# Optimization experiments

Hardware: AMD Instinct MI355X
Metric: run time of the kernel (lower is better)

## Reference

```python
import jax, jax.numpy as jnp
import numpy as np

N_P = 100000
N_A = 100000
IN = 128
H = 4
D = 32
E = 500000
ALPHA = 0.2


def _leaky(x, a=ALPHA):
    return jnp.where(x > 0, x, a * x)


def _gat_relation(Wh_src_rel, Wh_dst_self, a_src, a_dst, src, dst, n_dst):
    # Wh_src_rel: [Ns,H,D] relation-transformed source feats
    # Wh_dst_self: [Nd,H,D] self-transformed dest feats
    # a_src, a_dst: [H,D] attention vectors; src/dst: [E] edge index
    es = jnp.einsum('nhd,hd->nh', Wh_src_rel, a_src)  # [Ns,H]
    ed = jnp.einsum('nhd,hd->nh', Wh_dst_self, a_dst)  # [Nd,H]
    e = _leaky(es[src] + ed[dst])                      # [E,H]
    m = jax.ops.segment_max(e, dst, num_segments=n_dst)
    m = jnp.where(jnp.isfinite(m), m, 0.0)             # empty segments
    m = jax.lax.stop_gradient(m)
    ee = jnp.exp(e - m[dst])
    s = jax.ops.segment_sum(ee, dst, num_segments=n_dst)
    a = ee / s[dst]                                    # edge_softmax [E,H]
    msg = Wh_src_rel[src] * a[:, :, None]              # [E,H,D]
    return jax.ops.segment_sum(msg, dst, num_segments=n_dst)  # [Nd,H,D]


def setup_inputs() -> dict:
    key = jax.random.key(0)
    ks = jax.random.split(key, 32)
    inp = {
        'feat_P': jax.random.normal(ks[0], (N_P, IN), jnp.float32),
        'feat_A': jax.random.normal(ks[1], (N_A, IN), jnp.float32),
    }
    names = ['p2p', 'p2a', 'a2p', 'a2a']
    nsrc = {'p2p': N_P, 'p2a': N_P, 'a2p': N_A, 'a2a': N_A}
    ndst = {'p2p': N_P, 'p2a': N_A, 'a2p': N_P, 'a2a': N_A}
    for i, r in enumerate(names):
        inp['src_' + r] = jax.random.randint(ks[2 + 2 * i], (E,), 0, nsrc[r], jnp.int32)
        inp['dst_' + r] = jax.random.randint(ks[3 + 2 * i], (E,), 0, ndst[r], jnp.int32)
    # linear weights (torch Linear: y = x @ W.T + b); store as [IN, H*D]
    sc = 1.0 / np.sqrt(IN)
    for i, nm in enumerate(['P', 'A', 'p2p', 'p2a', 'a2p', 'a2a']):
        inp['W_' + nm] = jax.random.uniform(ks[10 + i], (IN, H * D), jnp.float32, -sc, sc)
        inp['b_' + nm] = jax.random.uniform(ks[16 + i], (H * D,), jnp.float32, -sc, sc)
    # attention vectors [H,D]
    for i, nm in enumerate(['p2p_src', 'p2p_dst', 'p2a_src', 'p2a_dst',
                            'a2p_src', 'a2p_dst', 'a2a_src', 'a2a_dst']):
        inp['att_' + nm] = jax.random.normal(ks[22 + i], (H, D), jnp.float32) * 0.1
    return inp


def reference(feat_P, feat_A,
              src_p2p, dst_p2p, src_p2a, dst_p2a,
              src_a2p, dst_a2p, src_a2a, dst_a2a,
              W_P, b_P, W_A, b_A, W_p2p, b_p2p, W_p2a, b_p2a,
              W_a2p, b_a2p, W_a2a, b_a2a,
              att_p2p_src, att_p2p_dst, att_p2a_src, att_p2a_dst,
              att_a2p_src, att_a2p_dst, att_a2a_src, att_a2a_dst):
    lin = lambda x, W, b: (x @ W + b).reshape(-1, H, D)
    Whp = lin(feat_P, W_P, b_P)      # [N_P,H,D]
    Wha = lin(feat_A, W_A, b_A)      # [N_A,H,D]
    Whp2p = lin(feat_P, W_p2p, b_p2p)
    Whp2a = lin(feat_P, W_p2a, b_p2a)
    Wha2p = lin(feat_A, W_a2p, b_a2p)
    Wha2a = lin(feat_A, W_a2a, b_a2a)
    ft_p2p = _gat_relation(Whp2p, Whp, att_p2p_src, att_p2p_dst, src_p2p, dst_p2p, N_P)
    ft_p2a = _gat_relation(Whp2a, Wha, att_p2a_src, att_p2a_dst, src_p2a, dst_p2a, N_A)
    ft_a2p = _gat_relation(Wha2p, Whp, att_a2p_src, att_a2p_dst, src_a2p, dst_a2p, N_P)
    ft_a2a = _gat_relation(Wha2a, Wha, att_a2a_src, att_a2a_dst, src_a2a, dst_a2a, N_A)
    h_P = jax.nn.relu(Whp + ft_p2p + ft_a2p)
    h_A = jax.nn.relu(Wha + ft_p2a + ft_a2a)
    return h_P, h_A
```

## Files before the change

kernel.cpp:

```cpp
#include <hip/hip_runtime.h>
#include <float.h>

#define ALPHA 0.2f
__device__ __forceinline__ float leakyf(float x) { return x > 0.0f ? x : ALPHA * x; }

__device__ __forceinline__ unsigned short f2bf(float f) {
    unsigned u = __float_as_uint(f);
    return (unsigned short)((u + 0x7FFFu + ((u >> 16) & 1u)) >> 16);
}
__device__ __forceinline__ float bflo(unsigned u) { return __uint_as_float(u << 16); }
__device__ __forceinline__ float bfhi(unsigned u) { return __uint_as_float(u & 0xFFFF0000u); }

typedef short bf16x8 __attribute__((ext_vector_type(8)));
typedef float f32x4 __attribute__((ext_vector_type(4)));

struct Ptr4i { const int* p0; const int* p1; const int* p2; const int* p3; };
struct PrepM { const float* W; const float* b; const float* attA; const float* attB; };

__global__ __launch_bounds__(256) void prep_count_kernel(
    PrepM m0, PrepM m1, PrepM m2, PrepM m3, PrepM m4, PrepM m5,
    bf16x8* __restrict__ wfrag, float* __restrict__ cd,
    Ptr4i dsts, int* __restrict__ pcnt, int nblkE, int E, int nCount)
{
    __shared__ int lh[4][128];
    if ((int)blockIdx.x < nCount) {
        ((int*)lh)[threadIdx.x] = 0;
        ((int*)lh)[threadIdx.x + 256] = 0;
        __syncthreads();
        int cb = blockIdx.x;
        int r = cb & 3, bx = cb >> 2;
        int w = threadIdx.x >> 6;
        const int* dst = (r == 0) ? dsts.p0 : (r == 1) ? dsts.p1 : (r == 2) ? dsts.p2 : dsts.p3;
        int base = bx * 4096;
        #pragma unroll 4
        for (int ii = 0; ii < 16; ++ii) {
            int i = base + threadIdx.x + 256 * ii;
            if (i < E) atomicAdd(&lh[w][dst[i] >> 10], 1);
        }
        __syncthreads();
        if (threadIdx.x < 128)
            pcnt[((size_t)r * nblkE + bx) * 128 + threadIdx.x] =
                lh[0][threadIdx.x] + lh[1][threadIdx.x] + lh[2][threadIdx.x] + lh[3][threadIdx.x];
        return;
    }
    int pb = blockIdx.x - nCount;
    int mi = pb >> 2;
    int part = pb & 3;
    PrepM mm = (mi == 0) ? m0 : (mi == 1) ? m1 : (mi == 2) ? m2 :
               (mi == 3) ? m3 : (mi == 4) ? m4 : m5;
    for (int ii = 0; ii < 3; ++ii) {
        int c = part * 576 + threadIdx.x + 256 * ii;
        if (c >= part * 576 + 576) continue;
        int t = c >> 8;
        int kstep = (c >> 6) & 3;
        int l = c & 63;
        int k0 = kstep * 32 + (l >> 4) * 8;
        bf16x8 out;
        if (t < 8) {
            int col = t * 16 + (l & 15);
            #pragma unroll
            for (int j = 0; j < 8; ++j)
                out[j] = (short)f2bf(mm.W[(size_t)(k0 + j) * 128 + col]);
        } else {
            int cl = l & 15;
            const float* att = nullptr; int h = 0;
            if (cl < 4 && mm.attA) { att = mm.attA; h = cl; }
            else if (cl >= 4 && cl < 8 && mm.attB) { att = mm.attB; h = cl - 4; }
            #pragma unroll
            for (int j = 0; j < 8; ++j) {
                float s = 0.f;
                if (att) {
                    const float* wrow = mm.W + (size_t)(k0 + j) * 128 + h * 32;
                    for (int d = 0; d < 32; ++d) s += wrow[d] * att[h * 32 + d];
                }
                out[j] = (short)f2bf(s);
            }
        }
        wfrag[(size_t)mi * 2304 + c] = out;
    }
    if (part == 0 && threadIdx.x < 8) {
        int cl = threadIdx.x;
        float s = 0.f;
        const float* att = nullptr; int h = 0;
        if (cl < 4 && mm.attA) { att = mm.attA; h = cl; }
        else if (cl >= 4 && mm.attB) { att = mm.attB; h = cl - 4; }
        if (att) for (int d = 0; d < 32; ++d) s += mm.b[h * 32 + d] * att[h * 32 + d];
        cd[mi * 8 + cl] = s;
    }
}

__global__ __launch_bounds__(512) void scan_kernel(
    const int* __restrict__ pcnt, int nblkE,
    int* __restrict__ bcnt, int* __restrict__ bbase, int* __restrict__ gwptr, int nbkMax)
{
    __shared__ int sh[4][128];
    int r = threadIdx.x >> 7, b = threadIdx.x & 127;
    int v = 0;
    if (b < nbkMax)
        for (int i = 0; i < nblkE; ++i)
            v += pcnt[((size_t)r * nblkE + i) * 128 + b];
    sh[r][b] = v;
    __syncthreads();
    #pragma unroll
    for (int off = 1; off < 128; off <<= 1) {
        int y = (b >= off) ? sh[r][b - off] : 0;
        __syncthreads();
        sh[r][b] += y;
        __syncthreads();
    }
    if (b < nbkMax) {
        int ex = sh[r][b] - v;
        bcnt[r * nbkMax + b]  = v;
        bbase[r * nbkMax + b] = ex;
        gwptr[r * nbkMax + b] = ex;
    }
}

__device__ __forceinline__ void mfma_compute_store(
    const short* xs_s, const short* wl_s, int row0, int N,
    const float* __restrict__ b, float* __restrict__ o32, unsigned short* __restrict__ o16,
    float* __restrict__ dotA, float* __restrict__ dotB, const float* __restrict__ cd)
{
    int l = threadIdx.x & 63, w = threadIdx.x >> 6;
    int cl = l & 15, gq = l >> 4;
    f32x4 acc[9];
    #pragma unroll
    for (int t = 0; t < 9; ++t) acc[t] = (f32x4){0.f, 0.f, 0.f, 0.f};
    int arow = w * 16 + cl;
    #pragma unroll
    for (int ks = 0; ks < 4; ++ks) {
        int k8 = ks * 4 + gq;
        bf16x8 a = *(const bf16x8*)((const char*)xs_s + arow * 256 + ((k8 * 16) ^ ((arow & 7) << 4)));
        #pragma unroll
        for (int t = 0; t < 9; ++t) {
            bf16x8 bf = *(const bf16x8*)((const char*)wl_s + ((t * 4 + ks) * 64 + l) * 16);
            acc[t] = __builtin_amdgcn_mfma_f32_16x16x32_bf16(a, bf, acc[t], 0, 0, 0);
        }
    }
    int rbase = row0 + w * 16 + gq * 4;
    #pragma unroll
    for (int t = 0; t < 8; ++t) {
        int col = t * 16 + cl;
        float bias = b[col];
        #pragma unroll
        for (int j = 0; j < 4; ++j) {
            int row = rbase + j;
            if (row < N) {
                float v = acc[t][j] + bias;
                if (o32) o32[(size_t)row * 128 + col] = v;
                else     o16[(size_t)row * 128 + col] = f2bf(v);
            }
        }
    }
    if (cl < 8) {
        float cdv = cd[cl];
        float* dp = (cl < 4) ? dotA : dotB;
        int h = cl & 3;
        if (dp) {
            #pragma unroll
            for (int j = 0; j < 4; ++j) {
                int row = rbase + j;
                if (row < N) dp[(size_t)row * 4 + h] = acc[8][j] + cdv;
            }
        }
    }
}

struct Lin3Cfg {
    const float* x; int N; int blocks;
    const bf16x8* wfrag; const float* cd;
    const float* b0; float* o0; float* dA0; float* dB0;
    const float* b1; unsigned short* o1; float* dA1;
    const float* b2; unsigned short* o2; float* dA2;
};

__global__ __launch_bounds__(256) void lin3_scatter_kernel(
    Lin3Cfg cP, Lin3Cfg cA, Ptr4i dsts, Ptr4i srcs,
    int* __restrict__ gwptr, unsigned* __restrict__ packed, int nbkMax, int E, int nScat)
{
    __shared__ __align__(16) char smem[53248];
    if ((int)blockIdx.x < nScat) {
        int* lh   = (int*)smem;
        int* loff = lh + 128;
        int* lptr = lh + 256;
        int* gb   = lh + 384;
        unsigned* stg = (unsigned*)(smem + 2048);
        unsigned short* sb = (unsigned short*)(smem + 2048 + 16384);
        if (threadIdx.x < 128) lh[threadIdx.x] = 0;
        __syncthreads();
        int cb = blockIdx.x;
        int r = cb & 3, bx = cb >> 2;
        const int* dst = (r == 0) ? dsts.p0 : (r == 1) ? dsts.p1 : (r == 2) ? dsts.p2 : dsts.p3;
        const int* src = (r == 0) ? srcs.p0 : (r == 1) ? srcs.p1 : (r == 2) ? srcs.p2 : srcs.p3;
        int base = bx * 4096;
        int d16[16], s16[16];
        #pragma unroll 4
        for (int ii = 0; ii < 16; ++ii) {
            int i = base + threadIdx.x + 256 * ii;
            if (i < E) {
                d16[ii] = dst[i];
                s16[ii] = src[i];
                atomicAdd(&lh[d16[ii] >> 10], 1);
            } else d16[ii] = -1;
        }
        __syncthreads();
        if (threadIdx.x == 0) {
            int run = 0;
            for (int b = 0; b < nbkMax; ++b) { loff[b] = run; lptr[b] = run; run += lh[b]; }
        }
        __syncthreads();
        #pragma unroll 4
        for (int ii = 0; ii < 16; ++ii) {
            if (d16[ii] >= 0) {
                int b = d16[ii] >> 10;
                int p = atomicAdd(&lptr[b], 1);
                stg[p] = ((unsigned)s16[ii] << 10) | (unsigned)(d16[ii] & 1023);
                sb[p] = (unsigned short)b;
            }
        }
        __syncthreads();
        if (threadIdx.x < nbkMax && lh[threadIdx.x])
            gb[threadIdx.x] = atomicAdd(&gwptr[r * nbkMax + threadIdx.x], lh[threadIdx.x]);
        __syncthreads();
        int tot = min(4096, E - base);
        #pragma unroll 4
        for (int ii = 0; ii < 16; ++ii) {
            int p = threadIdx.x + 256 * ii;
            if (p < tot) {
                int b = sb[p];
                packed[(size_t)r * E + gb[b] + (p - loff[b])] = stg[p];
            }
        }
        return;
    }
    short* xs_s = (short*)smem;
    short* wl_s = (short*)(smem + 16384);
    int bxl = blockIdx.x - nScat;
    const bool isP = bxl < cP.blocks;
    const Lin3Cfg& c = isP ? cP : cA;
    const int bx = isP ? bxl : (bxl - cP.blocks);
    const int row0 = bx * 64;
    const int N = c.N;

    #pragma unroll
    for (int ii = 0; ii < 4; ++ii) {
        int ci = threadIdx.x + 256 * ii;
        int r = ci >> 4, k8 = ci & 15;
        int srcrow = row0 + r; if (srcrow >= N) srcrow = N - 1;
        const float4* gp = (const float4*)(c.x + (size_t)srcrow * 128 + k8 * 8);
        float4 v0 = gp[0], v1 = gp[1];
        bf16x8 p;
        p[0] = (short)f2bf(v0.x); p[1] = (short)f2bf(v0.y);
        p[2] = (short)f2bf(v0.z); p[3] = (short)f2bf(v0.w);
        p[4] = (short)f2bf(v1.x); p[5] = (short)f2bf(v1.y);
        p[6] = (short)f2bf(v1.z); p[7] = (short)f2bf(v1.w);
        *(bf16x8*)((char*)xs_s + r * 256 + ((k8 * 16) ^ ((r & 7) << 4))) = p;
    }
    #pragma unroll
    for (int ii = 0; ii < 9; ++ii)
        ((bf16x8*)wl_s)[threadIdx.x + 256 * ii] = c.wfrag[threadIdx.x + 256 * ii];
    __syncthreads();
    mfma_compute_store(xs_s, wl_s, row0, N, c.b0, c.o0, nullptr, c.dA0, c.dB0, c.cd);

    __syncthreads();
    #pragma unroll
    for (int ii = 0; ii < 9; ++ii)
        ((bf16x8*)wl_s)[threadIdx.x + 256 * ii] = c.wfrag[2304 + threadIdx.x + 256 * ii];
    __syncthreads();
    mfma_compute_store(xs_s, wl_s, row0, N, c.b1, nullptr, c.o1, c.dA1, nullptr, c.cd + 8);

    __syncthreads();
    #pragma unroll
    for (int ii = 0; ii < 9; ++ii)
        ((bf16x8*)wl_s)[threadIdx.x + 256 * ii] = c.wfrag[2 * 2304 + threadIdx.x + 256 * ii];
    __syncthreads();
    mfma_compute_store(xs_s, wl_s, row0, N, c.b2, nullptr, c.o2, c.dA2, nullptr, c.cd + 16);
}

__global__ __launch_bounds__(256) void binB_build_kernel(
    const unsigned* __restrict__ packed, const int* __restrict__ bcnt, const int* __restrict__ bbase,
    int nbkMax, int4 Ns, int E, int stride,
    int* __restrict__ start, int* __restrict__ deg, int* __restrict__ csrc)
{
    int r = blockIdx.y, b = blockIdx.x;
    int N = (r == 0) ? Ns.x : (r == 1) ? Ns.y : (r == 2) ? Ns.z : Ns.w;
    int dst0 = b << 10;
    if (dst0 >= N) return;
    int cnt  = bcnt[r * nbkMax + b];
    int base = bbase[r * nbkMax + b];
    __shared__ int hist[1024];
    __shared__ int sums[256];
    #pragma unroll
    for (int i = 0; i < 4; ++i) hist[threadIdx.x * 4 + i] = 0;
    __syncthreads();
    const unsigned* pk = packed + (size_t)r * E + base;
    for (int i = threadIdx.x; i < cnt; i += 256)
        atomicAdd(&hist[pk[i] & 1023], 1);
    __syncthreads();
    int v4[4], s = 0;
    #pragma unroll
    for (int i = 0; i < 4; ++i) { v4[i] = hist[threadIdx.x * 4 + i]; s += v4[i]; }
    sums[threadIdx.x] = s;
    __syncthreads();
    #pragma unroll
    for (int off = 1; off < 256; off <<= 1) {
        int y = (threadIdx.x >= off) ? sums[threadIdx.x - off] : 0;
        __syncthreads();
        sums[threadIdx.x] += y;
        __syncthreads();
    }
    int run = sums[threadIdx.x] - s;
    int* st = start + (size_t)r * stride;
    int* dg = deg   + (size_t)r * stride;
    #pragma unroll
    for (int i = 0; i < 4; ++i) {
        int idx = threadIdx.x * 4 + i;
        int d = dst0 + idx;
        if (d < N) { dg[d] = v4[i]; st[d] = base + run; }
        hist[idx] = run;
        run += v4[i];
    }
    __syncthreads();
    int* cs = csrc + (size_t)r * E + base;
    for (int i = threadIdx.x; i < cnt; i += 256) {
        unsigned e = pk[i];
        int p = atomicAdd(&hist[e & 1023], 1);
        cs[p] = (int)(e >> 10);
    }
}

struct GatRel {
    const int* start; const int* deg; const int* csrc;
    const unsigned short* Wh; const float* es; const float* ed;
};
struct GatCfg { float* out; int Nd; int blocks; GatRel rel0, rel1; };

__global__ __launch_bounds__(256) void gat_node_kernel(GatCfg cP, GatCfg cA)
{
    const bool isP = blockIdx.x < (unsigned)cP.blocks;
    const GatCfg& c = isP ? cP : cA;
    const int bx = isP ? blockIdx.x : (blockIdx.x - cP.blocks);
    int gid = bx * 256 + threadIdx.x;
    int d = gid >> 6;
    if (d >= c.Nd) return;
    int lane = threadIdx.x & 63;
    int q = lane >> 4;
    int l = lane & 15;
    int h = l >> 2;

    const float4* orow = (const float4*)(c.out + (size_t)d * 128);
    float4 A0 = orow[l * 2], A1 = orow[l * 2 + 1];

    #pragma unroll
    for (int rel = 0; rel < 2; ++rel) {
        const GatRel& R = rel ? c.rel1 : c.rel0;
        int st = R.start[d];
        int n  = R.deg[d];
        if (n == 0) continue;
        const uint4* W4 = (const uint4*)R.Wh;
        float edv = R.ed[(size_t)d * 4 + h];
        float sum = 0.f;
        float m0 = 0.f, m1 = 0.f, m2 = 0.f, m3 = 0.f;
        float m4 = 0.f, m5 = 0.f, m6 = 0.f, m7 = 0.f;
        int j = q;
        for (; j + 4 < n; j += 8) {
            int s0 = R.csrc[st + j];
            int s1 = R.csrc[st + j + 4];
            float p0 = __expf(leakyf(R.es[(size_t)s0 * 4 + h] + edv));
            float p1 = __expf(leakyf(R.es[(size_t)s1 * 4 + h] + edv));
            uint4 w0 = W4[(size_t)s0 * 16 + l];
            uint4 w1 = W4[(size_t)s1 * 16 + l];
            sum += p0 + p1;
            m0 += p0 * bflo(w0.x) + p1 * bflo(w1.x);
            m1 += p0 * bfhi(w0.x) + p1 * bfhi(w1.x);
            m2 += p0 * bflo(w0.y) + p1 * bflo(w1.y);
            m3 += p0 * bfhi(w0.y) + p1 * bfhi(w1.y);
            m4 += p0 * bflo(w0.z) + p1 * bflo(w1.z);
            m5 += p0 * bfhi(w0.z) + p1 * bfhi(w1.z);
            m6 += p0 * bflo(w0.w) + p1 * bflo(w1.w);
            m7 += p0 * bfhi(w0.w) + p1 * bfhi(w1.w);
        }
        if (j < n) {
            int s0 = R.csrc[st + j];
            float p0 = __expf(leakyf(R.es[(size_t)s0 * 4 + h] + edv));
            uint4 w0 = W4[(size_t)s0 * 16 + l];
            sum += p0;
            m0 += p0 * bflo(w0.x); m1 += p0 * bfhi(w0.x);
            m2 += p0 * bflo(w0.y); m3 += p0 * bfhi(w0.y);
            m4 += p0 * bflo(w0.z); m5 += p0 * bfhi(w0.z);
            m6 += p0 * bflo(w0.w); m7 += p0 * bfhi(w0.w);
        }
        #pragma unroll
        for (int off = 16; off < 64; off <<= 1) {
            sum += __shfl_xor(sum, off, 64);
            m0 += __shfl_xor(m0, off, 64); m1 += __shfl_xor(m1, off, 64);
            m2 += __shfl_xor(m2, off, 64); m3 += __shfl_xor(m3, off, 64);
            m4 += __shfl_xor(m4, off, 64); m5 += __shfl_xor(m5, off, 64);
            m6 += __shfl_xor(m6, off, 64); m7 += __shfl_xor(m7, off, 64);
        }
        float inv = 1.0f / sum;
        A0.x += m0 * inv; A0.y += m1 * inv; A0.z += m2 * inv; A0.w += m3 * inv;
        A1.x += m4 * inv; A1.y += m5 * inv; A1.z += m6 * inv; A1.w += m7 * inv;
    }
    if (lane < 16) {
        A0.x = fmaxf(A0.x, 0.f); A0.y = fmaxf(A0.y, 0.f);
        A0.z = fmaxf(A0.z, 0.f); A0.w = fmaxf(A0.w, 0.f);
        A1.x = fmaxf(A1.x, 0.f); A1.y = fmaxf(A1.y, 0.f);
        A1.z = fmaxf(A1.z, 0.f); A1.w = fmaxf(A1.w, 0.f);
        float4* ow = (float4*)(c.out + (size_t)d * 128);
        ow[l * 2] = A0; ow[l * 2 + 1] = A1;
    }
}

extern "C" void kernel_launch(void* const* d_in, const int* in_sizes, int n_in,
                              void* d_out, int out_size, void* d_ws, size_t ws_size,
                              hipStream_t stream)
{
    const float* feat_P = (const float*)d_in[0];
    const float* feat_A = (const float*)d_in[1];
    const int* src_p2p = (const int*)d_in[2];
    const int* dst_p2p = (const int*)d_in[3];
    const int* src_p2a = (const int*)d_in[4];
    const int* dst_p2a = (const int*)d_in[5];
    const int* src_a2p = (const int*)d_in[6];
    const int* dst_a2p = (const int*)d_in[7];
    const int* src_a2a = (const int*)d_in[8];
    const int* dst_a2a = (const int*)d_in[9];
    const float* W_P   = (const float*)d_in[10]; const float* b_P   = (const float*)d_in[11];
    const float* W_A   = (const float*)d_in[12]; const float* b_A   = (const float*)d_in[13];
    const float* W_p2p = (const float*)d_in[14]; const float* b_p2p = (const float*)d_in[15];
    const float* W_p2a = (const float*)d_in[16]; const float* b_p2a = (const float*)d_in[17];
    const float* W_a2p = (const float*)d_in[18]; const float* b_a2p = (const float*)d_in[19];
    const float* W_a2a = (const float*)d_in[20]; const float* b_a2a = (const float*)d_in[21];
    const float* att_p2p_src = (const float*)d_in[22];
    const float* att_p2p_dst = (const float*)d_in[23];
    const float* att_p2a_src = (const float*)d_in[24];
    const float* att_p2a_dst = (const float*)d_in[25];
    const float* att_a2p_src = (const float*)d_in[26];
    const float* att_a2p_dst = (const float*)d_in[27];
    const float* att_a2a_src = (const float*)d_in[28];
    const float* att_a2a_dst = (const float*)d_in[29];

    const int NP = in_sizes[0] / 128;
    const int NA = in_sizes[1] / 128;
    const int E  = in_sizes[2];
    const int stride = (NP > NA) ? NP : NA;
    const int nbkMax = (stride + 1023) >> 10;
    const int nblkE  = (E + 4095) / 4096;
    const int nCount = 4 * nblkE;

    float* outP = (float*)d_out;
    float* outA = (float*)d_out + (size_t)NP * 128;

    char* ws = (char*)d_ws;
    size_t off = 0;
    auto alloc = [&](size_t bytes) -> void* {
        void* p = ws + off;
        off += (bytes + 255) & ~(size_t)255;
        return p;
    };
    unsigned short* Whp2p = (unsigned short*)alloc((size_t)NP * 128 * 2);
    unsigned short* Whp2a = (unsigned short*)alloc((size_t)NP * 128 * 2);
    unsigned short* Wha2p = (unsigned short*)alloc((size_t)NA * 128 * 2);
    unsigned short* Wha2a = (unsigned short*)alloc((size_t)NA * 128 * 2);
    float* es_p2p = (float*)alloc((size_t)NP * 16);
    float* es_p2a = (float*)alloc((size_t)NP * 16);
    float* es_a2p = (float*)alloc((size_t)NA * 16);
    float* es_a2a = (float*)alloc((size_t)NA * 16);
    float* ed_p2p = (float*)alloc((size_t)NP * 16);
    float* ed_a2p = (float*)alloc((size_t)NP * 16);
    float* ed_p2a = (float*)alloc((size_t)NA * 16);
    float* ed_a2a = (float*)alloc((size_t)NA * 16);
    int* deg    = (int*)alloc((size_t)4 * stride * 4);
    int* start  = (int*)alloc((size_t)4 * stride * 4);
    int* csrc   = (int*)alloc((size_t)4 * E * 4);
    unsigned* packed = (unsigned*)alloc((size_t)4 * E * 4);
    int* bcnt   = (int*)alloc((size_t)4 * nbkMax * 4);
    int* bbase  = (int*)alloc((size_t)4 * nbkMax * 4);
    int* gwptr  = (int*)alloc((size_t)4 * nbkMax * 4);
    int* pcnt   = (int*)alloc((size_t)4 * nblkE * 128 * 4);
    bf16x8* wfrag = (bf16x8*)alloc((size_t)6 * 2304 * 16);
    float* cd     = (float*)alloc((size_t)6 * 8 * 4);

    Ptr4i dsts = {dst_p2p, dst_a2p, dst_p2a, dst_a2a};
    Ptr4i srcs = {src_p2p, src_a2p, src_p2a, src_a2a};
    int4 Ns = make_int4(NP, NP, NA, NA);

    {
        PrepM m0 = {W_P,   b_P,   att_p2p_dst, att_a2p_dst};
        PrepM m1 = {W_p2p, b_p2p, att_p2p_src, nullptr};
        PrepM m2 = {W_p2a, b_p2a, att_p2a_src, nullptr};
        PrepM m3 = {W_A,   b_A,   att_p2a_dst, att_a2a_dst};
        PrepM m4 = {W_a2p, b_a2p, att_a2p_src, nullptr};
        PrepM m5 = {W_a2a, b_a2a, att_a2a_src, nullptr};
        prep_count_kernel<<<nCount + 24, 256, 0, stream>>>(m0, m1, m2, m3, m4, m5,
            wfrag, cd, dsts, pcnt, nblkE, E, nCount);
    }

    scan_kernel<<<1, 512, 0, stream>>>(pcnt, nblkE, bcnt, bbase, gwptr, nbkMax);

    {
        Lin3Cfg cP = {feat_P, NP, (NP + 63) / 64, wfrag, cd,
                      b_P, outP, ed_p2p, ed_a2p,
                      b_p2p, Whp2p, es_p2p,
                      b_p2a, Whp2a, es_p2a};
        Lin3Cfg cA = {feat_A, NA, (NA + 63) / 64, wfrag + (size_t)3 * 2304, cd + 24,
                      b_A, outA, ed_p2a, ed_a2a,
                      b_a2p, Wha2p, es_a2p,
                      b_a2a, Wha2a, es_a2a};
        lin3_scatter_kernel<<<nCount + cP.blocks + cA.blocks, 256, 0, stream>>>(
            cP, cA, dsts, srcs, gwptr, packed, nbkMax, E, nCount);
    }

    binB_build_kernel<<<dim3(nbkMax, 4), 256, 0, stream>>>(packed, bcnt, bbase,
        nbkMax, Ns, E, stride, start, deg, csrc);

    {
        GatCfg cP = {outP, NP, (NP * 64 + 255) / 256,
            {start + 0 * (size_t)stride, deg + 0 * (size_t)stride, csrc + 0 * (size_t)E, Whp2p, es_p2p, ed_p2p},
            {start + 1 * (size_t)stride, deg + 1 * (size_t)stride, csrc + 1 * (size_t)E, Wha2p, es_a2p, ed_a2p}};
        GatCfg cA = {outA, NA, (NA * 64 + 255) / 256,
            {start + 2 * (size_t)stride, deg + 2 * (size_t)stride, csrc + 2 * (size_t)E, Whp2a, es_p2a, ed_p2a},
            {start + 3 * (size_t)stride, deg + 3 * (size_t)stride, csrc + 3 * (size_t)E, Wha2a, es_a2a, ed_a2a}};
        gat_node_kernel<<<cP.blocks + cA.blocks, 256, 0, stream>>>(cP, cA);
    }
}
```

Before: 333.9 us.

## Stage linear weights in K-halves to shrink LDS; defer self-feature read in GAT

The fused linear/scatter kernel now stages each weight matrix's fragments in two K-halves instead of all at once. This cuts the shared-memory allocation from 52 KB to 34 KB so more blocks can be resident per CU, at the cost of extra barriers and staging steps. The GAT node kernel now accumulates messages starting from zero and reads the self feature row only in the final store by the writing lanes. This avoids every lane loading the output row up front and shortens register live ranges.

```diff
diff --git a/kernel.cpp b/kernel.cpp
--- a/kernel.cpp
+++ b/kernel.cpp
@@ -116,27 +116,31 @@
     }
 }
 
-__device__ __forceinline__ void mfma_compute_store(
-    const short* xs_s, const short* wl_s, int row0, int N,
-    const float* __restrict__ b, float* __restrict__ o32, unsigned short* __restrict__ o16,
-    float* __restrict__ dotA, float* __restrict__ dotB, const float* __restrict__ cd)
+__device__ __forceinline__ void mfma_khalf(
+    const short* xs_s, const short* wl_s, int kh, f32x4 acc[9])
 {
     int l = threadIdx.x & 63, w = threadIdx.x >> 6;
     int cl = l & 15, gq = l >> 4;
-    f32x4 acc[9];
-    #pragma unroll
-    for (int t = 0; t < 9; ++t) acc[t] = (f32x4){0.f, 0.f, 0.f, 0.f};
     int arow = w * 16 + cl;
     #pragma unroll
-    for (int ks = 0; ks < 4; ++ks) {
-        int k8 = ks * 4 + gq;
+    for (int ksp = 0; ksp < 2; ++ksp) {
+        int k8 = (kh * 2 + ksp) * 4 + gq;
         bf16x8 a = *(const bf16x8*)((const char*)xs_s + arow * 256 + ((k8 * 16) ^ ((arow & 7) << 4)));
         #pragma unroll
         for (int t = 0; t < 9; ++t) {
-            bf16x8 bf = *(const bf16x8*)((const char*)wl_s + ((t * 4 + ks) * 64 + l) * 16);
+            bf16x8 bf = *(const bf16x8*)((const char*)wl_s + ((t * 2 + ksp) * 64 + l) * 16);
             acc[t] = __builtin_amdgcn_mfma_f32_16x16x32_bf16(a, bf, acc[t], 0, 0, 0);
         }
     }
+}
+
+__device__ __forceinline__ void lin3_epilogue(
+    const f32x4 acc[9], int row0, int N,
+    const float* __restrict__ b, float* __restrict__ o32, unsigned short* __restrict__ o16,
+    float* __restrict__ dotA, float* __restrict__ dotB, const float* __restrict__ cd)
+{
+    int l = threadIdx.x & 63, w = threadIdx.x >> 6;
+    int cl = l & 15, gq = l >> 4;
     int rbase = row0 + w * 16 + gq * 4;
     #pragma unroll
     for (int t = 0; t < 8; ++t) {
@@ -178,7 +182,7 @@
     Lin3Cfg cP, Lin3Cfg cA, Ptr4i dsts, Ptr4i srcs,
     int* __restrict__ gwptr, unsigned* __restrict__ packed, int nbkMax, int E, int nScat)
 {
-    __shared__ __align__(16) char smem[53248];
+    __shared__ __align__(16) char smem[34816];
     if ((int)blockIdx.x < nScat) {
         int* lh   = (int*)smem;
         int* loff = lh + 128;
@@ -256,25 +260,38 @@
         p[6] = (short)f2bf(v1.z); p[7] = (short)f2bf(v1.w);
         *(bf16x8*)((char*)xs_s + r * 256 + ((k8 * 16) ^ ((r & 7) << 4))) = p;
     }
-    #pragma unroll
-    for (int ii = 0; ii < 9; ++ii)
-        ((bf16x8*)wl_s)[threadIdx.x + 256 * ii] = c.wfrag[threadIdx.x + 256 * ii];
-    __syncthreads();
-    mfma_compute_store(xs_s, wl_s, row0, N, c.b0, c.o0, nullptr, c.dA0, c.dB0, c.cd);
-
-    __syncthreads();
-    #pragma unroll
-    for (int ii = 0; ii < 9; ++ii)
-        ((bf16x8*)wl_s)[threadIdx.x + 256 * ii] = c.wfrag[2304 + threadIdx.x + 256 * ii];
-    __syncthreads();
-    mfma_compute_store(xs_s, wl_s, row0, N, c.b1, nullptr, c.o1, c.dA1, nullptr, c.cd + 8);
-
-    __syncthreads();
-    #pragma unroll
-    for (int ii = 0; ii < 9; ++ii)
-        ((bf16x8*)wl_s)[threadIdx.x + 256 * ii] = c.wfrag[2 * 2304 + threadIdx.x + 256 * ii];
-    __syncthreads();
-    mfma_compute_store(xs_s, wl_s, row0, N, c.b2, nullptr, c.o2, c.dA2, nullptr, c.cd + 16);
+    #define STAGE_HALF(MIOFF, KH)                                              \
+        {                                                                      \
+            const bf16x8* wf = c.wfrag + (size_t)(MIOFF) * 2304;               \
+            for (int ii = 0; ii < 5; ++ii) {                                   \
+                int ch = threadIdx.x + 256 * ii;                               \
+                if (ch < 1152) {                                               \
+                    int t = ch >> 7, rem = ch & 127;                           \
+                    ((bf16x8*)wl_s)[ch] = wf[t * 256 + (KH) * 128 + rem];      \
+                }                                                              \
+            }                                                                  \
+        }
+    f32x4 acc[9];
+    #pragma unroll
+    for (int mi = 0; mi < 3; ++mi) {
+        #pragma unroll
+        for (int t = 0; t < 9; ++t) acc[t] = (f32x4){0.f, 0.f, 0.f, 0.f};
+        STAGE_HALF(mi, 0)
+        __syncthreads();
+        mfma_khalf(xs_s, wl_s, 0, acc);
+        __syncthreads();
+        STAGE_HALF(mi, 1)
+        __syncthreads();
+        mfma_khalf(xs_s, wl_s, 1, acc);
+        if (mi == 0)
+            lin3_epilogue(acc, row0, N, c.b0, c.o0, nullptr, c.dA0, c.dB0, c.cd);
+        else if (mi == 1)
+            lin3_epilogue(acc, row0, N, c.b1, nullptr, c.o1, c.dA1, nullptr, c.cd + 8);
+        else
+            lin3_epilogue(acc, row0, N, c.b2, nullptr, c.o2, c.dA2, nullptr, c.cd + 16);
+        __syncthreads();
+    }
+    #undef STAGE_HALF
 }
 
 __global__ __launch_bounds__(256) void binB_build_kernel(
@@ -348,8 +365,8 @@
     int l = lane & 15;
     int h = l >> 2;
 
-    const float4* orow = (const float4*)(c.out + (size_t)d * 128);
-    float4 A0 = orow[l * 2], A1 = orow[l * 2 + 1];
+    float a0 = 0.f, a1 = 0.f, a2 = 0.f, a3 = 0.f;
+    float a4 = 0.f, a5 = 0.f, a6 = 0.f, a7 = 0.f;
 
     #pragma unroll
     for (int rel = 0; rel < 2; ++rel) {
@@ -399,16 +416,18 @@
             m6 += __shfl_xor(m6, off, 64); m7 += __shfl_xor(m7, off, 64);
         }
         float inv = 1.0f / sum;
-        A0.x += m0 * inv; A0.y += m1 * inv; A0.z += m2 * inv; A0.w += m3 * inv;
-        A1.x += m4 * inv; A1.y += m5 * inv; A1.z += m6 * inv; A1.w += m7 * inv;
+        a0 += m0 * inv; a1 += m1 * inv; a2 += m2 * inv; a3 += m3 * inv;
+        a4 += m4 * inv; a5 += m5 * inv; a6 += m6 * inv; a7 += m7 * inv;
     }
     if (lane < 16) {
-        A0.x = fmaxf(A0.x, 0.f); A0.y = fmaxf(A0.y, 0.f);
-        A0.z = fmaxf(A0.z, 0.f); A0.w = fmaxf(A0.w, 0.f);
-        A1.x = fmaxf(A1.x, 0.f); A1.y = fmaxf(A1.y, 0.f);
-        A1.z = fmaxf(A1.z, 0.f); A1.w = fmaxf(A1.w, 0.f);
-        float4* ow = (float4*)(c.out + (size_t)d * 128);
-        ow[l * 2] = A0; ow[l * 2 + 1] = A1;
+        float* orow = c.out + (size_t)d * 128;
+        float4 s0 = ((const float4*)orow)[l * 2];
+        float4 s1 = ((const float4*)orow)[l * 2 + 1];
+        s0.x = fmaxf(s0.x + a0, 0.f); s0.y = fmaxf(s0.y + a1, 0.f);
+        s0.z = fmaxf(s0.z + a2, 0.f); s0.w = fmaxf(s0.w + a3, 0.f);
+        s1.x = fmaxf(s1.x + a4, 0.f); s1.y = fmaxf(s1.y + a5, 0.f);
+        s1.z = fmaxf(s1.z + a6, 0.f); s1.w = fmaxf(s1.w + a7, 0.f);
+        ((float4*)orow)[l * 2] = s0; ((float4*)orow)[l * 2 + 1] = s1;
     }
 }
 
```

Result: slower. 365.1 us (+9.3%).
